# Kernel optimization log

Measured on AMD Instinct MI355X. Metric: run time of the kernel, lower is better.

The kernel has to match this reference:

```python
import jax, jax.numpy as jnp
import numpy as np

N_NODES = 100000
N_EDGES = 625000
D_IN = 128
D_OUT = 128
N_ETYPES = 64


def setup_inputs() -> dict:
    key = jax.random.key(0)
    k1, k2, k3, k4, k5, k6 = jax.random.split(key, 6)
    node_features = jax.random.normal(k1, (N_NODES, D_IN), dtype=jnp.float32)
    edge_index = jax.random.randint(k2, (2, N_EDGES), 0, N_NODES, dtype=jnp.int64)
    edge_type = jax.random.randint(k3, (N_EDGES,), 0, N_ETYPES, dtype=jnp.int64)
    edge_emb = jax.random.normal(k4, (N_ETYPES, D_OUT), dtype=jnp.float32)
    W = jax.random.normal(k5, (D_IN, D_OUT), dtype=jnp.float32) / np.sqrt(D_IN)
    b = jax.random.normal(k6, (D_OUT,), dtype=jnp.float32) * 0.01
    return {"node_features": node_features, "edge_index": edge_index,
            "edge_type": edge_type, "edge_emb": edge_emb, "W": W, "b": b}


def reference(node_features, edge_index, edge_type, edge_emb, W, b):
    # Linear transform of node features: (N, D_out)
    h = node_features @ W + b
    src, tgt = edge_index[0], edge_index[1]
    # Per-edge message: gather src feature + edge-type embedding  (E, D_out)
    messages = h[src] + edge_emb[edge_type]
    # Scatter-add into target nodes
    aggregated = jax.ops.segment_sum(messages, tgt, num_segments=N_NODES)
    # Self contribution + ReLU
    return jax.nn.relu(aggregated + h)
```

## Files before the change

### kernel.cpp

```cpp
#include <hip/hip_runtime.h>
#include <hip/hip_bf16.h>

#define D 128

typedef __attribute__((ext_vector_type(8))) short short8v;
typedef __attribute__((ext_vector_type(4))) float float4v;

__device__ __forceinline__ unsigned short f2bf(float f) {
  union { float f; unsigned int u; } v; v.f = f;
  unsigned int r = v.u + 0x7fffu + ((v.u >> 16) & 1u);
  return (unsigned short)(r >> 16);
}
__device__ __forceinline__ float bf2f(unsigned int bits16) {
  union { unsigned int u; float f; } v; v.u = bits16 << 16;
  return v.f;
}

__global__ __launch_bounds__(256) void prep_kernel(
    const float* __restrict__ W, const float* __restrict__ eemb,
    unsigned short* __restrict__ Wt, unsigned short* __restrict__ em_bf) {
  int i = blockIdx.x * 256 + threadIdx.x;
  if (i < D * D) Wt[i] = f2bf(W[(i & 127) * D + (i >> 7)]);
  if (i < 64 * D) em_bf[i] = f2bf(eemb[i]);
}

#define XS_STRIDE 138
__global__ __launch_bounds__(256) void gemm_h_kernel(
    const float* __restrict__ nf, const unsigned short* __restrict__ Wt,
    const float* __restrict__ b, unsigned short* __restrict__ h_bf,
    int n_nodes) {
  __shared__ unsigned short Xs[64 * XS_STRIDE];
  const int tid = threadIdx.x;
  const int nodeBase = blockIdx.x * 64;

  #pragma unroll
  for (int s = 0; s < 4; ++s) {
    const int row = (tid >> 4) + s * 16;
    const int col = (tid & 15) * 8;
    short8v sv;
    if (nodeBase + row < n_nodes) {
      const float4* p = (const float4*)&nf[(size_t)(nodeBase + row) * D + col];
      float4 a = p[0], c = p[1];
      sv[0] = (short)f2bf(a.x); sv[1] = (short)f2bf(a.y);
      sv[2] = (short)f2bf(a.z); sv[3] = (short)f2bf(a.w);
      sv[4] = (short)f2bf(c.x); sv[5] = (short)f2bf(c.y);
      sv[6] = (short)f2bf(c.z); sv[7] = (short)f2bf(c.w);
    } else {
      sv = short8v{0, 0, 0, 0, 0, 0, 0, 0};
    }
    *(short8v*)&Xs[row * XS_STRIDE + col] = sv;
  }

  const int w = tid >> 6;
  const int l = tid & 63;
  const int m = l & 15;
  const int q = l >> 4;
  const int n0 = (w & 1) * 64;
  const int nodeHalf = (w >> 1) * 32;

  short8v afrag[4][4];
  #pragma unroll
  for (int nt = 0; nt < 4; ++nt) {
    const int n = n0 + nt * 16 + m;
    #pragma unroll
    for (int kc = 0; kc < 4; ++kc)
      afrag[nt][kc] = *(const short8v*)&Wt[n * D + kc * 32 + q * 8];
  }

  float4v acc[4][2] = {};
  __syncthreads();

  #pragma unroll
  for (int kc = 0; kc < 4; ++kc) {
    #pragma unroll
    for (int t = 0; t < 2; ++t) {
      const int node = nodeHalf + t * 16 + m;
      const short8v bv =
          *(const short8v*)&Xs[node * XS_STRIDE + kc * 32 + q * 8];
      #pragma unroll
      for (int nt = 0; nt < 4; ++nt)
        acc[nt][t] = __builtin_amdgcn_mfma_f32_16x16x32_bf16(
            afrag[nt][kc], bv, acc[nt][t], 0, 0, 0);
    }
  }

  #pragma unroll
  for (int nt = 0; nt < 4; ++nt) {
    const int colBase = n0 + nt * 16 + q * 4;
    const float4 bv = *(const float4*)&b[colBase];
    #pragma unroll
    for (int t = 0; t < 2; ++t) {
      const int node = nodeBase + nodeHalf + t * 16 + m;
      if (node < n_nodes) {
        const unsigned int lo = (unsigned int)f2bf(acc[nt][t][0] + bv.x) |
                                ((unsigned int)f2bf(acc[nt][t][1] + bv.y) << 16);
        const unsigned int hi = (unsigned int)f2bf(acc[nt][t][2] + bv.z) |
                                ((unsigned int)f2bf(acc[nt][t][3] + bv.w) << 16);
        uint2 val; val.x = lo; val.y = hi;
        *(uint2*)&h_bf[(size_t)node * D + colBase] = val;
      }
    }
  }
}

__global__ __launch_bounds__(256) void hist_kernel(
    const int* __restrict__ eidx, int* __restrict__ counts, int n_edges) {
  int e = blockIdx.x * 256 + threadIdx.x;
  if (e < n_edges) atomicAdd(&counts[eidx[n_edges + e]], 1);
}

__global__ __launch_bounds__(256) void scan1_kernel(
    const int* __restrict__ counts, int* __restrict__ offsets,
    int* __restrict__ blockSums, int n) {
  __shared__ int lds[256];
  const int tid = threadIdx.x;
  const int base = blockIdx.x * 1024 + tid * 4;
  int v[4];
  #pragma unroll
  for (int k = 0; k < 4; ++k) v[k] = (base + k < n) ? counts[base + k] : 0;
  int s = v[0] + v[1] + v[2] + v[3];
  lds[tid] = s;
  for (int off = 1; off < 256; off <<= 1) {
    __syncthreads();
    int t = (tid >= off) ? lds[tid - off] : 0;
    __syncthreads();
    lds[tid] += t;
  }
  __syncthreads();
  int run = lds[tid] - s;
  #pragma unroll
  for (int k = 0; k < 4; ++k) {
    if (base + k < n) offsets[base + k] = run;
    run += v[k];
  }
  if (tid == 255) blockSums[blockIdx.x] = lds[255];
}

__global__ __launch_bounds__(1024) void scan2_kernel(int* __restrict__ blockSums,
                                                     int* __restrict__ blockOffs,
                                                     int nb) {
  __shared__ int lds[1024];
  const int tid = threadIdx.x;
  int v = (tid < nb) ? blockSums[tid] : 0;
  lds[tid] = v;
  for (int off = 1; off < 1024; off <<= 1) {
    __syncthreads();
    int t = (tid >= off) ? lds[tid - off] : 0;
    __syncthreads();
    lds[tid] += t;
  }
  __syncthreads();
  if (tid < nb) blockOffs[tid] = lds[tid] - v;
}

__global__ __launch_bounds__(256) void scan3_kernel(
    int* __restrict__ offsets, int* __restrict__ cursor,
    const int* __restrict__ blockOffs, int n, int n_edges) {
  const int tid = threadIdx.x;
  const int add = blockOffs[blockIdx.x];
  const int base = blockIdx.x * 1024 + tid * 4;
  #pragma unroll
  for (int k = 0; k < 4; ++k) {
    int i = base + k;
    if (i < n) {
      int o = offsets[i] + add;
      offsets[i] = o;
      cursor[i] = o;
    }
  }
  if (blockIdx.x == 0 && tid == 0) offsets[n] = n_edges;
}

__global__ __launch_bounds__(256) void scatter_kernel(
    const int* __restrict__ eidx, const int* __restrict__ etype,
    int* __restrict__ cursor, unsigned int* __restrict__ packed, int n_edges) {
  int e = blockIdx.x * 256 + threadIdx.x;
  if (e >= n_edges) return;
  const int src = eidx[e];
  const int tgt = eidx[n_edges + e];
  const int et = etype[e];
  const int pos = atomicAdd(&cursor[tgt], 1);
  packed[pos] = (unsigned int)src | ((unsigned int)et << 17);
}

__global__ __launch_bounds__(256) void aggregate_kernel(
    const int* __restrict__ offsets, const unsigned int* __restrict__ packed,
    const unsigned int* __restrict__ em, const unsigned int* __restrict__ h2,
    float* __restrict__ out, int n_nodes) {
  const int gid = blockIdx.x * 256 + threadIdx.x;
  const int n = gid >> 6;
  const int lane = gid & 63;
  if (n >= n_nodes) return;

  const unsigned int sb = h2[n * 64 + lane];
  float ax0 = bf2f(sb & 0xffffu), ay0 = bf2f(sb >> 16);
  float ax1 = 0.f, ay1 = 0.f;

  int j = offsets[n];
  const int end = offsets[n + 1];
  for (; j + 3 < end; j += 4) {
    const unsigned int p0 = packed[j];
    const unsigned int p1 = packed[j + 1];
    const unsigned int p2 = packed[j + 2];
    const unsigned int p3 = packed[j + 3];
    const unsigned int g0 = h2[(p0 & 0x1FFFFu) * 64 + lane];
    const unsigned int g1 = h2[(p1 & 0x1FFFFu) * 64 + lane];
    const unsigned int g2 = h2[(p2 & 0x1FFFFu) * 64 + lane];
    const unsigned int g3 = h2[(p3 & 0x1FFFFu) * 64 + lane];
    const unsigned int e0 = em[(p0 >> 17) * 64 + lane];
    const unsigned int e1 = em[(p1 >> 17) * 64 + lane];
    const unsigned int e2 = em[(p2 >> 17) * 64 + lane];
    const unsigned int e3 = em[(p3 >> 17) * 64 + lane];
    ax0 += bf2f(g0 & 0xffffu) + bf2f(e0 & 0xffffu);
    ay0 += bf2f(g0 >> 16) + bf2f(e0 >> 16);
    ax1 += bf2f(g1 & 0xffffu) + bf2f(e1 & 0xffffu);
    ay1 += bf2f(g1 >> 16) + bf2f(e1 >> 16);
    ax0 += bf2f(g2 & 0xffffu) + bf2f(e2 & 0xffffu);
    ay0 += bf2f(g2 >> 16) + bf2f(e2 >> 16);
    ax1 += bf2f(g3 & 0xffffu) + bf2f(e3 & 0xffffu);
    ay1 += bf2f(g3 >> 16) + bf2f(e3 >> 16);
  }
  for (; j < end; ++j) {
    const unsigned int p0 = packed[j];
    const unsigned int g0 = h2[(p0 & 0x1FFFFu) * 64 + lane];
    const unsigned int e0 = em[(p0 >> 17) * 64 + lane];
    ax0 += bf2f(g0 & 0xffffu) + bf2f(e0 & 0xffffu);
    ay0 += bf2f(g0 >> 16) + bf2f(e0 >> 16);
  }
  float2 r;
  r.x = fmaxf(ax0 + ax1, 0.f);
  r.y = fmaxf(ay0 + ay1, 0.f);
  ((float2*)out)[(size_t)n * 64 + lane] = r;
}

extern "C" void kernel_launch(void* const* d_in, const int* in_sizes, int n_in,
                              void* d_out, int out_size, void* d_ws,
                              size_t ws_size, hipStream_t stream) {
  const float* nf   = (const float*)d_in[0];
  const int*   eidx = (const int*)d_in[1];
  const int*   etyp = (const int*)d_in[2];
  const float* eemb = (const float*)d_in[3];
  const float* W    = (const float*)d_in[4];
  const float* b    = (const float*)d_in[5];

  const int n_nodes = in_sizes[0] / D;
  const int n_edges = in_sizes[2];

  float* out = (float*)d_out;

  char* base = (char*)d_ws;
  unsigned short* Wt = (unsigned short*)base;
  unsigned short* em_bf = (unsigned short*)(base + 32768);
  unsigned short* h_bf = (unsigned short*)(base + 49152);
  int* counts = (int*)(base + 49152 + (size_t)n_nodes * D * 2);
  int* offsets = counts + n_nodes;
  int* cursor = offsets + (n_nodes + 1);
  int* blockSums = cursor + n_nodes;
  int* blockOffs = blockSums + 1024;
  unsigned int* packed = (unsigned int*)(blockOffs + 1024);

  const int nb = (n_nodes + 1023) / 1024;

  prep_kernel<<<64, 256, 0, stream>>>(W, eemb, Wt, em_bf);

  gemm_h_kernel<<<(n_nodes + 63) / 64, 256, 0, stream>>>(nf, Wt, b, h_bf,
                                                         n_nodes);

  (void)hipMemsetAsync(counts, 0, (size_t)n_nodes * 4, stream);
  hist_kernel<<<(n_edges + 255) / 256, 256, 0, stream>>>(eidx, counts, n_edges);
  scan1_kernel<<<nb, 256, 0, stream>>>(counts, offsets, blockSums, n_nodes);
  scan2_kernel<<<1, 1024, 0, stream>>>(blockSums, blockOffs, nb);
  scan3_kernel<<<nb, 256, 0, stream>>>(offsets, cursor, blockOffs, n_nodes,
                                       n_edges);
  scatter_kernel<<<(n_edges + 255) / 256, 256, 0, stream>>>(eidx, etyp, cursor,
                                                            packed, n_edges);

  const long long aggThreads = (long long)n_nodes * 64;
  aggregate_kernel<<<(int)((aggThreads + 255) / 256), 256, 0, stream>>>(
      offsets, packed, (const unsigned int*)em_bf, (const unsigned int*)h_bf,
      out, n_nodes);
}
```

Before: 154.2 us.

## Process two nodes per wavefront with 8-byte gathers and zero-row padding

The aggregate kernel now gives each node 32 lanes instead of 64, so each wavefront handles two nodes and each lane gathers a uint2 (four bf16 values). Padding entries point at zero-filled sentinel rows appended to h and the edge embeddings, which lets the loop run a uniform trip count per half-wave with no scalar tail. The bf16 conversions switch to packed intrinsics in the GEMM, and the workspace layout shifts to make room for the sentinel rows. The intent is to cut wave count and per-edge instruction overhead and to issue wider memory requests. The cost is wasted gathers whenever the two nodes in a wave have unequal degrees.

```diff
diff --git a/kernel.cpp b/kernel.cpp
--- a/kernel.cpp
+++ b/kernel.cpp
@@ -11,17 +11,28 @@
   unsigned int r = v.u + 0x7fffu + ((v.u >> 16) & 1u);
   return (unsigned short)(r >> 16);
 }
-__device__ __forceinline__ float bf2f(unsigned int bits16) {
-  union { unsigned int u; float f; } v; v.u = bits16 << 16;
-  return v.f;
+__device__ __forceinline__ unsigned int pkbf(float lo, float hi) {
+  float2 f; f.x = lo; f.y = hi;
+  __hip_bfloat162 v = __float22bfloat162_rn(f);
+  union { __hip_bfloat162 b; unsigned int u; } c; c.b = v;
+  return c.u;
+}
+__device__ __forceinline__ float bflo(unsigned int u) {
+  union { unsigned int v; float f; } c; c.v = u << 16; return c.f;
+}
+__device__ __forceinline__ float bfhi(unsigned int u) {
+  union { unsigned int v; float f; } c; c.v = u & 0xffff0000u; return c.f;
 }
 
 __global__ __launch_bounds__(256) void prep_kernel(
     const float* __restrict__ W, const float* __restrict__ eemb,
-    unsigned short* __restrict__ Wt, unsigned short* __restrict__ em_bf) {
+    unsigned short* __restrict__ Wt, unsigned short* __restrict__ em_bf,
+    unsigned short* __restrict__ h_bf, int n_nodes) {
   int i = blockIdx.x * 256 + threadIdx.x;
   if (i < D * D) Wt[i] = f2bf(W[(i & 127) * D + (i >> 7)]);
   if (i < 64 * D) em_bf[i] = f2bf(eemb[i]);
+  if (i < 64) ((unsigned int*)(h_bf + (size_t)n_nodes * D))[i] = 0u;
+  if (i >= 64 && i < 128) ((unsigned int*)(em_bf + 64 * D))[i - 64] = 0u;
 }
 
 #define XS_STRIDE 138
@@ -37,18 +48,16 @@
   for (int s = 0; s < 4; ++s) {
     const int row = (tid >> 4) + s * 16;
     const int col = (tid & 15) * 8;
-    short8v sv;
+    uint4 sv = {0u, 0u, 0u, 0u};
     if (nodeBase + row < n_nodes) {
       const float4* p = (const float4*)&nf[(size_t)(nodeBase + row) * D + col];
       float4 a = p[0], c = p[1];
-      sv[0] = (short)f2bf(a.x); sv[1] = (short)f2bf(a.y);
-      sv[2] = (short)f2bf(a.z); sv[3] = (short)f2bf(a.w);
-      sv[4] = (short)f2bf(c.x); sv[5] = (short)f2bf(c.y);
-      sv[6] = (short)f2bf(c.z); sv[7] = (short)f2bf(c.w);
-    } else {
-      sv = short8v{0, 0, 0, 0, 0, 0, 0, 0};
-    }
-    *(short8v*)&Xs[row * XS_STRIDE + col] = sv;
+      sv.x = pkbf(a.x, a.y);
+      sv.y = pkbf(a.z, a.w);
+      sv.z = pkbf(c.x, c.y);
+      sv.w = pkbf(c.z, c.w);
+    }
+    *(uint4*)&Xs[row * XS_STRIDE + col] = sv;
   }
 
   const int w = tid >> 6;
@@ -92,11 +101,9 @@
     for (int t = 0; t < 2; ++t) {
       const int node = nodeBase + nodeHalf + t * 16 + m;
       if (node < n_nodes) {
-        const unsigned int lo = (unsigned int)f2bf(acc[nt][t][0] + bv.x) |
-                                ((unsigned int)f2bf(acc[nt][t][1] + bv.y) << 16);
-        const unsigned int hi = (unsigned int)f2bf(acc[nt][t][2] + bv.z) |
-                                ((unsigned int)f2bf(acc[nt][t][3] + bv.w) << 16);
-        uint2 val; val.x = lo; val.y = hi;
+        uint2 val;
+        val.x = pkbf(acc[nt][t][0] + bv.x, acc[nt][t][1] + bv.y);
+        val.y = pkbf(acc[nt][t][2] + bv.z, acc[nt][t][3] + bv.w);
         *(uint2*)&h_bf[(size_t)node * D + colBase] = val;
       }
     }
@@ -185,52 +192,60 @@
 
 __global__ __launch_bounds__(256) void aggregate_kernel(
     const int* __restrict__ offsets, const unsigned int* __restrict__ packed,
-    const unsigned int* __restrict__ em, const unsigned int* __restrict__ h2,
-    float* __restrict__ out, int n_nodes) {
+    const uint2* __restrict__ e4, const uint2* __restrict__ h4,
+    float* __restrict__ out, int n_nodes, int n_edges, unsigned int zero_p) {
   const int gid = blockIdx.x * 256 + threadIdx.x;
-  const int n = gid >> 6;
-  const int lane = gid & 63;
+  const int lane = threadIdx.x & 63;
+  const int half = lane >> 5;
+  const int sl = lane & 31;
+  const int n = (gid >> 6) * 2 + half;
   if (n >= n_nodes) return;
 
-  const unsigned int sb = h2[n * 64 + lane];
-  float ax0 = bf2f(sb & 0xffffu), ay0 = bf2f(sb >> 16);
-  float ax1 = 0.f, ay1 = 0.f;
+  const uint2 sb = h4[(size_t)n * 32 + sl];
+  float a0 = bflo(sb.x), a1 = bfhi(sb.x), a2 = bflo(sb.y), a3 = bfhi(sb.y);
+  float c0 = 0.f, c1 = 0.f, c2 = 0.f, c3 = 0.f;
 
   int j = offsets[n];
   const int end = offsets[n + 1];
-  for (; j + 3 < end; j += 4) {
-    const unsigned int p0 = packed[j];
-    const unsigned int p1 = packed[j + 1];
-    const unsigned int p2 = packed[j + 2];
-    const unsigned int p3 = packed[j + 3];
-    const unsigned int g0 = h2[(p0 & 0x1FFFFu) * 64 + lane];
-    const unsigned int g1 = h2[(p1 & 0x1FFFFu) * 64 + lane];
-    const unsigned int g2 = h2[(p2 & 0x1FFFFu) * 64 + lane];
-    const unsigned int g3 = h2[(p3 & 0x1FFFFu) * 64 + lane];
-    const unsigned int e0 = em[(p0 >> 17) * 64 + lane];
-    const unsigned int e1 = em[(p1 >> 17) * 64 + lane];
-    const unsigned int e2 = em[(p2 >> 17) * 64 + lane];
-    const unsigned int e3 = em[(p3 >> 17) * 64 + lane];
-    ax0 += bf2f(g0 & 0xffffu) + bf2f(e0 & 0xffffu);
-    ay0 += bf2f(g0 >> 16) + bf2f(e0 >> 16);
-    ax1 += bf2f(g1 & 0xffffu) + bf2f(e1 & 0xffffu);
-    ay1 += bf2f(g1 >> 16) + bf2f(e1 >> 16);
-    ax0 += bf2f(g2 & 0xffffu) + bf2f(e2 & 0xffffu);
-    ay0 += bf2f(g2 >> 16) + bf2f(e2 >> 16);
-    ax1 += bf2f(g3 & 0xffffu) + bf2f(e3 & 0xffffu);
-    ay1 += bf2f(g3 >> 16) + bf2f(e3 >> 16);
-  }
-  for (; j < end; ++j) {
-    const unsigned int p0 = packed[j];
-    const unsigned int g0 = h2[(p0 & 0x1FFFFu) * 64 + lane];
-    const unsigned int e0 = em[(p0 >> 17) * 64 + lane];
-    ax0 += bf2f(g0 & 0xffffu) + bf2f(e0 & 0xffffu);
-    ay0 += bf2f(g0 >> 16) + bf2f(e0 >> 16);
-  }
-  float2 r;
-  r.x = fmaxf(ax0 + ax1, 0.f);
-  r.y = fmaxf(ay0 + ay1, 0.f);
-  ((float2*)out)[(size_t)n * 64 + lane] = r;
+  int trips = (end - j + 3) >> 2;
+  int to = __shfl_xor(trips, 32);
+  const int T = trips > to ? trips : to;
+  const int emax = n_edges - 1;
+
+  for (int t = 0; t < T; ++t, j += 4) {
+    const int j1 = j + 1, j2 = j + 2, j3 = j + 3;
+    unsigned int p0 = packed[j  <= emax ? j  : emax];
+    unsigned int p1 = packed[j1 <= emax ? j1 : emax];
+    unsigned int p2 = packed[j2 <= emax ? j2 : emax];
+    unsigned int p3 = packed[j3 <= emax ? j3 : emax];
+    p0 = (j  < end) ? p0 : zero_p;
+    p1 = (j1 < end) ? p1 : zero_p;
+    p2 = (j2 < end) ? p2 : zero_p;
+    p3 = (j3 < end) ? p3 : zero_p;
+    const uint2 g0 = h4[(size_t)(p0 & 0x1FFFFu) * 32 + sl];
+    const uint2 g1 = h4[(size_t)(p1 & 0x1FFFFu) * 32 + sl];
+    const uint2 g2 = h4[(size_t)(p2 & 0x1FFFFu) * 32 + sl];
+    const uint2 g3 = h4[(size_t)(p3 & 0x1FFFFu) * 32 + sl];
+    const uint2 e0 = e4[(p0 >> 17) * 32 + sl];
+    const uint2 e1 = e4[(p1 >> 17) * 32 + sl];
+    const uint2 e2 = e4[(p2 >> 17) * 32 + sl];
+    const uint2 e3 = e4[(p3 >> 17) * 32 + sl];
+    a0 += bflo(g0.x) + bflo(e0.x); a1 += bfhi(g0.x) + bfhi(e0.x);
+    a2 += bflo(g0.y) + bflo(e0.y); a3 += bfhi(g0.y) + bfhi(e0.y);
+    c0 += bflo(g1.x) + bflo(e1.x); c1 += bfhi(g1.x) + bfhi(e1.x);
+    c2 += bflo(g1.y) + bflo(e1.y); c3 += bfhi(g1.y) + bfhi(e1.y);
+    a0 += bflo(g2.x) + bflo(e2.x); a1 += bfhi(g2.x) + bfhi(e2.x);
+    a2 += bflo(g2.y) + bflo(e2.y); a3 += bfhi(g2.y) + bfhi(e2.y);
+    c0 += bflo(g3.x) + bflo(e3.x); c1 += bfhi(g3.x) + bfhi(e3.x);
+    c2 += bflo(g3.y) + bflo(e3.y); c3 += bfhi(g3.y) + bfhi(e3.y);
+  }
+
+  float4 r;
+  r.x = fmaxf(a0 + c0, 0.f);
+  r.y = fmaxf(a1 + c1, 0.f);
+  r.z = fmaxf(a2 + c2, 0.f);
+  r.w = fmaxf(a3 + c3, 0.f);
+  ((float4*)out)[(size_t)n * 32 + sl] = r;
 }
 
 extern "C" void kernel_launch(void* const* d_in, const int* in_sizes, int n_in,
@@ -251,8 +266,9 @@
   char* base = (char*)d_ws;
   unsigned short* Wt = (unsigned short*)base;
   unsigned short* em_bf = (unsigned short*)(base + 32768);
-  unsigned short* h_bf = (unsigned short*)(base + 49152);
-  int* counts = (int*)(base + 49152 + (size_t)n_nodes * D * 2);
+  unsigned short* h_bf = (unsigned short*)(base + 65536);
+  char* tail = base + 65536 + (size_t)(n_nodes + 1) * D * 2;
+  int* counts = (int*)tail;
   int* offsets = counts + n_nodes;
   int* cursor = offsets + (n_nodes + 1);
   int* blockSums = cursor + n_nodes;
@@ -261,7 +277,7 @@
 
   const int nb = (n_nodes + 1023) / 1024;
 
-  prep_kernel<<<64, 256, 0, stream>>>(W, eemb, Wt, em_bf);
+  prep_kernel<<<64, 256, 0, stream>>>(W, eemb, Wt, em_bf, h_bf, n_nodes);
 
   gemm_h_kernel<<<(n_nodes + 63) / 64, 256, 0, stream>>>(nf, Wt, b, h_bf,
                                                          n_nodes);
@@ -275,8 +291,9 @@
   scatter_kernel<<<(n_edges + 255) / 256, 256, 0, stream>>>(eidx, etyp, cursor,
                                                             packed, n_edges);
 
-  const long long aggThreads = (long long)n_nodes * 64;
-  aggregate_kernel<<<(int)((aggThreads + 255) / 256), 256, 0, stream>>>(
-      offsets, packed, (const unsigned int*)em_bf, (const unsigned int*)h_bf,
-      out, n_nodes);
-}
+  const unsigned int zero_p = (unsigned int)n_nodes | (64u << 17);
+  const int aggBlocks = (n_nodes + 7) / 8;
+  aggregate_kernel<<<aggBlocks, 256, 0, stream>>>(
+      offsets, packed, (const uint2*)em_bf, (const uint2*)h_bf, out, n_nodes,
+      n_edges, zero_p);
+}
```

Result: faster. 148.1 us (-3.9%).
